# Optimization experiments

Measured on AMD Instinct MI355X. Metric: run time of the kernel, lower is better.

## Reference

```python
import jax, jax.numpy as jnp
import numpy as np

B, L, D = 8, 64, 768
F, P, A = 50, 49, 49   # frames, patches, attention dim
N, C = 20000, 36       # grid points, grid_size**2 cells
LN_EPS = 1e-12


def setup_inputs() -> dict:
    key = jax.random.key(0)
    ks = jax.random.split(key, 16)
    s = 0.02
    return {
        "lang": jax.random.normal(ks[0], (B, L, D), jnp.float32),
        "lang_cls": jax.random.normal(ks[1], (B, A), jnp.float32),
        "frames": jax.random.normal(ks[2], (B, F, P, A), jnp.float32),
        "candidates": jax.random.normal(ks[3], (B, C, 2), jnp.float32),
        "grid_fts": jax.random.normal(ks[4], (B, N, D), jnp.float32),
        "grid_index": jax.random.randint(ks[5], (B, N), 0, C, jnp.int32),
        # SoftDotAttention params (bias=False in torch)
        "W_in": jax.random.normal(ks[6], (A, A), jnp.float32) * s,
        "W_out": jax.random.normal(ks[7], (A, 2 * A), jnp.float32) * s,
        # fc2: 49 -> demb
        "W_fc2": jax.random.normal(ks[8], (D, A), jnp.float32) * s,
        "b_fc2": jnp.zeros((D,), jnp.float32),
        # text_proj / grid_proj: 768 -> 768
        "W_text": jax.random.normal(ks[9], (D, D), jnp.float32) * s,
        "b_text": jnp.zeros((D,), jnp.float32),
        "W_grid": jax.random.normal(ks[10], (D, D), jnp.float32) * s,
        "b_grid": jnp.zeros((D,), jnp.float32),
        # candidate_encoder: Linear(2, demb) + LayerNorm(demb)
        "W_cand": jax.random.normal(ks[11], (D, 2), jnp.float32) * s,
        "b_cand": jnp.zeros((D,), jnp.float32),
        "ln_g": jnp.ones((D,), jnp.float32),
        "ln_b": jnp.zeros((D,), jnp.float32),
    }


def reference(lang, lang_cls, frames, candidates, grid_fts, grid_index,
              W_in, W_out, W_fc2, b_fc2, W_text, b_text, W_grid, b_grid,
              W_cand, b_cand, ln_g, ln_b):
    # ---- SoftDotAttention over every frame (vectorized over F) ----
    target = lang_cls @ W_in.T                                  # [B,A]
    attn = jnp.einsum('bfpa,ba->bfp', frames, target)           # [B,F,P]
    attn = jax.nn.softmax(attn, axis=-1)
    wctx = jnp.einsum('bfp,bfpa->bfa', attn, frames)            # [B,F,A]
    h = jnp.broadcast_to(lang_cls[:, None, :], wctx.shape)      # [B,F,A]
    att_frame = jnp.tanh(jnp.concatenate([wctx, h], -1) @ W_out.T)  # [B,F,A]
    emb_frames = att_frame @ W_fc2.T + b_fc2                    # [B,F,D]

    # ---- grid segment softmax-reduce ----
    text = lang @ W_text.T + b_text                             # [B,L,D]
    # score of each grid point = max over language tokens
    w = jnp.einsum('bnd,bld->bnl', grid_fts, text).max(-1)      # [B,N]
    g = grid_fts @ W_grid.T + b_grid                            # [B,N,D]
    mask = grid_index[..., None] == jnp.arange(C)[None, None]   # [B,N,C]
    logits = jnp.where(mask, w[..., None], -jnp.inf)            # [B,N,C]
    m = logits.max(axis=1, keepdims=True)                       # [B,1,C]
    m = jnp.where(jnp.isfinite(m), m, 0.0)
    e = jnp.where(mask, jnp.exp(logits - m), 0.0)
    den = e.sum(axis=1, keepdims=True)                          # [B,1,C]
    p = jnp.where(den > 0, e / jnp.maximum(den, 1e-30), 0.0)    # [B,N,C]
    grid_map = jnp.einsum('bnc,bnd->bcd', p, g)                 # [B,C,D]

    # ---- candidate encoder: Linear + LayerNorm, scaled by lang[:, :1, :] ----
    c = candidates @ W_cand.T + b_cand                          # [B,C,D]
    mu = c.mean(-1, keepdims=True)
    var = ((c - mu) ** 2).mean(-1, keepdims=True)
    c = (c - mu) * jax.lax.rsqrt(var + LN_EPS) * ln_g + ln_b
    emb_cand = c * lang[:, :1, :] + grid_map                    # [B,C,D]

    return jnp.concatenate([emb_frames, emb_cand], axis=1)      # [B,F+C,D]
```

## Files before the change

### kernel.cpp

```cpp
#include <hip/hip_runtime.h>
#include <math.h>

#define Bh 8
#define Lh 64
#define Dh 768
#define Fh 50
#define Ph 49
#define Ah 49
#define Nh 20000
#define Ch 36
#define CAP 2048
#define NCH 8
#define CUTE 2e-6f

typedef __bf16 bf16x8 __attribute__((ext_vector_type(8)));
typedef float f32x4 __attribute__((ext_vector_type(4)));
union U { uint4 u; bf16x8 v; };

__device__ __forceinline__ void cvt2(float a0, float a1, unsigned& h, unsigned& l) {
    unsigned u0 = __float_as_uint(a0), u1 = __float_as_uint(a1);
    unsigned h0 = u0 & 0xFFFF0000u, h1 = u1 & 0xFFFF0000u;
    h = (h0 >> 16) | h1;
    float l0 = a0 - __uint_as_float(h0);
    float l1 = a1 - __uint_as_float(h1);
    l = (__float_as_uint(l0) >> 16) | (__float_as_uint(l1) & 0xFFFF0000u);
}

__device__ __forceinline__ void cvt8(float4 p, float4 q, bf16x8& h8, bf16x8& l8) {
    U h, l;
    cvt2(p.x, p.y, h.u.x, l.u.x);
    cvt2(p.z, p.w, h.u.y, l.u.y);
    cvt2(q.x, q.y, h.u.z, l.u.z);
    cvt2(q.z, q.w, h.u.w, l.u.w);
    h8 = h.v; l8 = l.v;
}

__device__ __forceinline__ float dec_max(unsigned u) {
    if (u == 0u) return 0.f;
    return (u & 0x80000000u) ? __uint_as_float(u ^ 0x80000000u) : __uint_as_float(~u);
}

__global__ __launch_bounds__(256) void k_prep(const float* __restrict__ Wg,
                                              const float* __restrict__ Wt,
                                              const float* __restrict__ Wf2,
                                              uint4* __restrict__ WgH, uint4* __restrict__ WgL,
                                              uint4* __restrict__ WtH, uint4* __restrict__ WtL,
                                              float* __restrict__ Wf2T,
                                              unsigned* __restrict__ m_u,
                                              float* __restrict__ den,
                                              int* __restrict__ cnt) {
    int bx = blockIdx.x, tid = threadIdx.x;
    if (bx < 576) {
        bool g = bx < 288;
        int gid = (g ? bx : bx - 288) * 256 + tid;
        const float* W = g ? Wg : Wt;
        int l = gid & 63;
        int rest = gid >> 6;
        int ct = rest % 48, ks = rest / 48;
        const float* src = W + (size_t)(ct * 16 + (l & 15)) * Dh + ks * 32 + (l >> 4) * 8;
        float4 p = *(const float4*)src;
        float4 q = *(const float4*)(src + 4);
        U h, lo;
        cvt2(p.x, p.y, h.u.x, lo.u.x);
        cvt2(p.z, p.w, h.u.y, lo.u.y);
        cvt2(q.x, q.y, h.u.z, lo.u.z);
        cvt2(q.z, q.w, h.u.w, lo.u.w);
        if (g) { WgH[gid] = h.u; WgL[gid] = lo.u; }
        else   { WtH[gid] = h.u; WtL[gid] = lo.u; }
    } else if (bx < 723) {
        int i = (bx - 576) * 256 + tid;
        int d = i / 49, j = i - d * 49;
        Wf2T[j * Dh + d] = Wf2[i];
    } else {
        for (int i = tid; i < Bh * Ch; i += 256) { m_u[i] = 0u; den[i] = 0.f; cnt[i] = 0; }
    }
}

__global__ __launch_bounds__(256) void k_tf(const float* __restrict__ lang,
                                            const uint4* __restrict__ WtH,
                                            const uint4* __restrict__ WtL,
                                            const float* __restrict__ bt,
                                            const float* __restrict__ frames,
                                            const float* __restrict__ lang_cls,
                                            const float* __restrict__ W_in,
                                            const float* __restrict__ W_out,
                                            const float* __restrict__ Wf2T,
                                            const float* __restrict__ b_fc2,
                                            float* __restrict__ text,
                                            float* __restrict__ out) {
    __shared__ float smem[8192];
    int bx = blockIdx.x;
    int tid = threadIdx.x;

    if (bx < 48) {
        float (*lds)[4096] = (float(*)[4096])smem;
        int wv = tid >> 6, l = tid & 63;
        int dt = bx % 12;
        int m0 = (bx / 12) * 128;

        const uint4* pbh = WtH + (size_t)dt * 256 + l;
        const uint4* pbl = WtL + (size_t)dt * 256 + l;

        const float* srcA[4]; int dA[4];
#pragma unroll
        for (int r = 0; r < 4; ++r) {
            int s = r * 256 + tid, row = s >> 3, pos = s & 7;
            srcA[r] = lang + (size_t)(m0 + row) * Dh + pos * 4;
            dA[r] = row * 32 + ((pos ^ (row & 7)) << 2);
        }
        int lm = l & 15, lh = l >> 4, r7 = lm & 7;
        int oA[2][2];
#pragma unroll
        for (int rt = 0; rt < 2; ++rt)
#pragma unroll
            for (int j = 0; j < 2; ++j)
                oA[rt][j] = (wv * 32 + rt * 16 + lm) * 32 + (((lh * 2 + j) ^ r7) << 2);

        {
            float4 v0 = *(const float4*)srcA[0];
            float4 v1 = *(const float4*)srcA[1];
            float4 v2 = *(const float4*)srcA[2];
            float4 v3 = *(const float4*)srcA[3];
            *(float4*)&lds[0][dA[0]] = v0;
            *(float4*)&lds[0][dA[1]] = v1;
            *(float4*)&lds[0][dA[2]] = v2;
            *(float4*)&lds[0][dA[3]] = v3;
        }
        __syncthreads();

        f32x4 acc[2][4];
#pragma unroll
        for (int i = 0; i < 2; ++i)
#pragma unroll
            for (int j = 0; j < 4; ++j) acc[i][j] = (f32x4){0.f, 0.f, 0.f, 0.f};

        for (int t = 0; t < 24; ++t) {
            int cur = t & 1;
            float4 p0, p1, p2, p3;
            bool pf = (t < 23);
            if (pf) {
                int o = (t + 1) * 32;
                p0 = *(const float4*)(srcA[0] + o);
                p1 = *(const float4*)(srcA[1] + o);
                p2 = *(const float4*)(srcA[2] + o);
                p3 = *(const float4*)(srcA[3] + o);
            }
            uint4 bh0 = pbh[t * 3072 +   0], bh1 = pbh[t * 3072 +  64];
            uint4 bh2 = pbh[t * 3072 + 128], bh3 = pbh[t * 3072 + 192];
            uint4 bl0 = pbl[t * 3072 +   0], bl1 = pbl[t * 3072 +  64];
            uint4 bl2 = pbl[t * 3072 + 128], bl3 = pbl[t * 3072 + 192];

            const float* L = lds[cur];
            float4 a00 = *(const float4*)&L[oA[0][0]];
            float4 a01 = *(const float4*)&L[oA[0][1]];
            float4 a10 = *(const float4*)&L[oA[1][0]];
            float4 a11 = *(const float4*)&L[oA[1][1]];
            bf16x8 ah0, al0, ah1, al1;
            cvt8(a00, a01, ah0, al0);
            cvt8(a10, a11, ah1, al1);

            uint4 bhu[4] = {bh0, bh1, bh2, bh3};
            uint4 blu[4] = {bl0, bl1, bl2, bl3};
#pragma unroll
            for (int ct = 0; ct < 4; ++ct) {
                U ubh, ubl; ubh.u = bhu[ct]; ubl.u = blu[ct];
                bf16x8 bh = ubh.v, bl = ubl.v;
                acc[0][ct] = __builtin_amdgcn_mfma_f32_16x16x32_bf16(ah0, bh, acc[0][ct], 0, 0, 0);
                acc[0][ct] = __builtin_amdgcn_mfma_f32_16x16x32_bf16(al0, bh, acc[0][ct], 0, 0, 0);
                acc[0][ct] = __builtin_amdgcn_mfma_f32_16x16x32_bf16(ah0, bl, acc[0][ct], 0, 0, 0);
                acc[1][ct] = __builtin_amdgcn_mfma_f32_16x16x32_bf16(ah1, bh, acc[1][ct], 0, 0, 0);
                acc[1][ct] = __builtin_amdgcn_mfma_f32_16x16x32_bf16(al1, bh, acc[1][ct], 0, 0, 0);
                acc[1][ct] = __builtin_amdgcn_mfma_f32_16x16x32_bf16(ah1, bl, acc[1][ct], 0, 0, 0);
            }
            if (pf) {
                float* D = lds[cur ^ 1];
                *(float4*)&D[dA[0]] = p0;
                *(float4*)&D[dA[1]] = p1;
                *(float4*)&D[dA[2]] = p2;
                *(float4*)&D[dA[3]] = p3;
            }
            __syncthreads();
        }

#pragma unroll
        for (int rt = 0; rt < 2; ++rt) {
#pragma unroll
            for (int r = 0; r < 4; ++r) {
                int row = m0 + wv * 32 + rt * 16 + lh * 4 + r;
#pragma unroll
                for (int ct = 0; ct < 4; ++ct) {
                    int d = dt * 64 + ct * 16 + lm;
                    text[(size_t)row * Dh + d] = acc[rt][ct][r] + bt[d];
                }
            }
        }
    } else {
        int fid = bx - 48;
        int b = fid / Fh, f = fid % Fh;
        float* fr = smem;
        float* tg = smem + 2401;
        float* cl = smem + 2450;
        float* at = smem + 2499;
        float* wc = smem + 2548;
        float* af = smem + 2597;
        const float* fp = frames + ((size_t)(b * Fh + f)) * (Ph * Ah);
        for (int i = tid; i < Ph * Ah; i += 256) fr[i] = fp[i];
        if (tid < Ah) {
            cl[tid] = lang_cls[b * Ah + tid];
            float s = 0.f;
            for (int k = 0; k < Ah; ++k) s += lang_cls[b * Ah + k] * W_in[tid * Ah + k];
            tg[tid] = s;
        }
        __syncthreads();
        if (tid < Ph) {
            float s = 0.f;
            for (int a = 0; a < Ah; ++a) s += fr[tid * Ah + a] * tg[a];
            at[tid] = s;
        }
        __syncthreads();
        if (tid < 64) {
            float raw = (tid < Ph) ? at[tid] : -3.4e38f;
            float v = raw;
            for (int m = 32; m; m >>= 1) v = fmaxf(v, __shfl_xor(v, m));
            float e = (tid < Ph) ? expf(raw - v) : 0.f;
            float s = e;
            for (int m = 32; m; m >>= 1) s += __shfl_xor(s, m);
            if (tid < Ph) at[tid] = e / s;
        }
        __syncthreads();
        if (tid < Ah) {
            float s = 0.f;
            for (int p = 0; p < Ph; ++p) s += at[p] * fr[p * Ah + tid];
            wc[tid] = s;
        }
        __syncthreads();
        if (tid < Ah) {
            float s = 0.f;
            for (int a = 0; a < Ah; ++a)
                s += wc[a] * W_out[tid * (2 * Ah) + a] + cl[a] * W_out[tid * (2 * Ah) + Ah + a];
            af[tid] = tanhf(s);
        }
        __syncthreads();
        for (int d = tid; d < Dh; d += 256) {
            float s = b_fc2[d];
            for (int j = 0; j < Ah; ++j) s += af[j] * Wf2T[j * Dh + d];
            out[((size_t)(b * (Fh + Ch) + f)) * Dh + d] = s;
        }
    }
}

__global__ __launch_bounds__(256) void k_tfrag(const float* __restrict__ text,
                                               uint4* __restrict__ textH,
                                               uint4* __restrict__ textL) {
    int gid = blockIdx.x * 256 + threadIdx.x;
    int l  = gid & 63;
    int ct = (gid >> 6) & 3;
    int bk = gid >> 8;
    int b  = bk / 24, ks = bk % 24;
    const float* src = text + ((size_t)(b * Lh + ct * 16 + (l & 15))) * Dh
                     + ks * 32 + (l >> 4) * 8;
    float4 p = *(const float4*)src;
    float4 q = *(const float4*)(src + 4);
    U h, lo;
    cvt2(p.x, p.y, h.u.x, lo.u.x);
    cvt2(p.z, p.w, h.u.y, lo.u.y);
    cvt2(q.x, q.y, h.u.z, lo.u.z);
    cvt2(q.z, q.w, h.u.w, lo.u.w);
    textH[gid] = h.u;
    textL[gid] = lo.u;
}

__global__ __launch_bounds__(256) void k_w(const float* __restrict__ grid,
                                           const uint4* __restrict__ textH,
                                           const uint4* __restrict__ textL,
                                           const int* __restrict__ gi,
                                           float* __restrict__ w,
                                           unsigned* __restrict__ m_u) {
    __shared__ float lds[2][4096];
    __shared__ unsigned mu[Ch];
    int b = blockIdx.y;
    int tid = threadIdx.x;
    int wv = tid >> 6, l = tid & 63;
    int n0 = blockIdx.x * 128;
    if (tid < Ch) mu[tid] = 0u;

    const float* gb = grid + (size_t)b * Nh * Dh;
    const uint4* pbh = textH + (size_t)b * 6144 + l;
    const uint4* pbl = textL + (size_t)b * 6144 + l;

    const float* srcA[4]; int dA[4];
#pragma unroll
    for (int r = 0; r < 4; ++r) {
        int s = r * 256 + tid, row = s >> 3, pos = s & 7;
        int rowg = n0 + row; if (rowg >= Nh) rowg = Nh - 1;
        srcA[r] = gb + (size_t)rowg * Dh + pos * 4;
        dA[r] = row * 32 + ((pos ^ (row & 7)) << 2);
    }
    int lm = l & 15, lh = l >> 4, r7 = lm & 7;
    int oA[2][2];
#pragma unroll
    for (int rt = 0; rt < 2; ++rt)
#pragma unroll
        for (int j = 0; j < 2; ++j)
            oA[rt][j] = (wv * 32 + rt * 16 + lm) * 32 + (((lh * 2 + j) ^ r7) << 2);

    {
        float4 v0 = *(const float4*)srcA[0];
        float4 v1 = *(const float4*)srcA[1];
        float4 v2 = *(const float4*)srcA[2];
        float4 v3 = *(const float4*)srcA[3];
        *(float4*)&lds[0][dA[0]] = v0;
        *(float4*)&lds[0][dA[1]] = v1;
        *(float4*)&lds[0][dA[2]] = v2;
        *(float4*)&lds[0][dA[3]] = v3;
    }
    __syncthreads();

    f32x4 acc[2][4];
#pragma unroll
    for (int i = 0; i < 2; ++i)
#pragma unroll
        for (int j = 0; j < 4; ++j) acc[i][j] = (f32x4){0.f, 0.f, 0.f, 0.f};

    for (int t = 0; t < 24; ++t) {
        int cur = t & 1;
        float4 p0, p1, p2, p3;
        bool pf = (t < 23);
        if (pf) {
            int o = (t + 1) * 32;
            p0 = *(const float4*)(srcA[0] + o);
            p1 = *(const float4*)(srcA[1] + o);
            p2 = *(const float4*)(srcA[2] + o);
            p3 = *(const float4*)(srcA[3] + o);
        }
        uint4 bh0 = pbh[t * 256 +   0], bh1 = pbh[t * 256 +  64];
        uint4 bh2 = pbh[t * 256 + 128], bh3 = pbh[t * 256 + 192];
        uint4 bl0 = pbl[t * 256 +   0], bl1 = pbl[t * 256 +  64];
        uint4 bl2 = pbl[t * 256 + 128], bl3 = pbl[t * 256 + 192];

        const float* L = lds[cur];
        float4 a00 = *(const float4*)&L[oA[0][0]];
        float4 a01 = *(const float4*)&L[oA[0][1]];
        float4 a10 = *(const float4*)&L[oA[1][0]];
        float4 a11 = *(const float4*)&L[oA[1][1]];
        bf16x8 ah0, al0, ah1, al1;
        cvt8(a00, a01, ah0, al0);
        cvt8(a10, a11, ah1, al1);

        uint4 bhu[4] = {bh0, bh1, bh2, bh3};
        uint4 blu[4] = {bl0, bl1, bl2, bl3};
#pragma unroll
        for (int ct = 0; ct < 4; ++ct) {
            U ubh, ubl; ubh.u = bhu[ct]; ubl.u = blu[ct];
            bf16x8 bh = ubh.v, bl = ubl.v;
            acc[0][ct] = __builtin_amdgcn_mfma_f32_16x16x32_bf16(ah0, bh, acc[0][ct], 0, 0, 0);
            acc[0][ct] = __builtin_amdgcn_mfma_f32_16x16x32_bf16(al0, bh, acc[0][ct], 0, 0, 0);
            acc[0][ct] = __builtin_amdgcn_mfma_f32_16x16x32_bf16(ah0, bl, acc[0][ct], 0, 0, 0);
            acc[1][ct] = __builtin_amdgcn_mfma_f32_16x16x32_bf16(ah1, bh, acc[1][ct], 0, 0, 0);
            acc[1][ct] = __builtin_amdgcn_mfma_f32_16x16x32_bf16(al1, bh, acc[1][ct], 0, 0, 0);
            acc[1][ct] = __builtin_amdgcn_mfma_f32_16x16x32_bf16(ah1, bl, acc[1][ct], 0, 0, 0);
        }
        if (pf) {
            float* D = lds[cur ^ 1];
            *(float4*)&D[dA[0]] = p0;
            *(float4*)&D[dA[1]] = p1;
            *(float4*)&D[dA[2]] = p2;
            *(float4*)&D[dA[3]] = p3;
        }
        __syncthreads();
    }

#pragma unroll
    for (int rt = 0; rt < 2; ++rt) {
        float m[4];
#pragma unroll
        for (int r = 0; r < 4; ++r) {
            m[r] = fmaxf(fmaxf(acc[rt][0][r], acc[rt][1][r]),
                         fmaxf(acc[rt][2][r], acc[rt][3][r]));
            m[r] = fmaxf(m[r], __shfl_xor(m[r], 1));
            m[r] = fmaxf(m[r], __shfl_xor(m[r], 2));
            m[r] = fmaxf(m[r], __shfl_xor(m[r], 4));
            m[r] = fmaxf(m[r], __shfl_xor(m[r], 8));
        }
        if (lm == 0) {
#pragma unroll
            for (int r = 0; r < 4; ++r) {
                int row = n0 + wv * 32 + rt * 16 + lh * 4 + r;
                if (row < Nh) {
                    w[b * Nh + row] = m[r];
                    unsigned u = __float_as_uint(m[r]);
                    u = (u & 0x80000000u) ? ~u : (u | 0x80000000u);
                    atomicMax(&mu[gi[b * Nh + row]], u);
                }
            }
        }
    }
    __syncthreads();
    if (tid < Ch && mu[tid]) atomicMax(&m_u[b * Ch + tid], mu[tid]);
}

__global__ __launch_bounds__(256) void k_epc(const float* __restrict__ w,
                                             const int* __restrict__ gi,
                                             const unsigned* __restrict__ m_u,
                                             float* __restrict__ den,
                                             int* __restrict__ cnt,
                                             int* __restrict__ bn,
                                             float* __restrict__ bp) {
    int b = blockIdx.y;
    int n = blockIdx.x * 256 + threadIdx.x;
    __shared__ float dn[Ch];
    if (threadIdx.x < Ch) dn[threadIdx.x] = 0.f;
    __syncthreads();
    if (n < Nh) {
        int c = gi[b * Nh + n];
        float e = expf(w[b * Nh + n] - dec_max(m_u[b * Ch + c]));
        atomicAdd(&dn[c], e);
        if (e > CUTE) {
            int pos = atomicAdd(&cnt[b * Ch + c], 1);
            if (pos < CAP) {
                bn[(b * Ch + c) * CAP + pos] = n;
                bp[(b * Ch + c) * CAP + pos] = e;
            }
        }
    }
    __syncthreads();
    if (threadIdx.x < Ch && dn[threadIdx.x] != 0.f)
        atomicAdd(&den[b * Ch + threadIdx.x], dn[threadIdx.x]);
}

__global__ __launch_bounds__(256) void k_S3(const float* __restrict__ grid,
                                            const int* __restrict__ cnt,
                                            const int* __restrict__ bn,
                                            const float* __restrict__ bp,
                                            float* __restrict__ Spart) {
    int c = blockIdx.x, dq = blockIdx.y;
    int b = blockIdx.z >> 3, ch = blockIdx.z & 7;
    int d = dq * 256 + threadIdx.x;
    int len = cnt[b * Ch + c]; if (len > CAP) len = CAP;
    int i0 = ch * (CAP / NCH);
    int i1 = i0 + (CAP / NCH); if (i1 > len) i1 = len;
    size_t base = (size_t)(b * Ch + c) * CAP;
    size_t po = ((size_t)(b * Ch + c) * NCH + ch) * Dh + d;
    const float* gb = grid + (size_t)b * Nh * Dh + d;
    float a[8] = {0.f, 0.f, 0.f, 0.f, 0.f, 0.f, 0.f, 0.f};
    int i = i0;
    for (; i + 8 <= i1; i += 8) {
        int nn[8]; float pp[8];
#pragma unroll
        for (int j = 0; j < 8; ++j) { nn[j] = bn[base + i + j]; pp[j] = bp[base + i + j]; }
#pragma unroll
        for (int j = 0; j < 8; ++j) a[j] += pp[j] * gb[(size_t)nn[j] * Dh];
    }
    for (; i < i1; ++i) a[0] += bp[base + i] * gb[(size_t)bn[base + i] * Dh];
    Spart[po] = ((a[0] + a[1]) + (a[2] + a[3])) + ((a[4] + a[5]) + (a[6] + a[7]));
}

__global__ __launch_bounds__(256) void k_red(const float* __restrict__ Spart,
                                             float* __restrict__ S) {
    int bc = blockIdx.x, dq = blockIdx.y;
    int d = dq * 256 + threadIdx.x;
    float s = 0.f;
#pragma unroll
    for (int ch = 0; ch < NCH; ++ch)
        s += Spart[((size_t)bc * NCH + ch) * Dh + d];
    S[(size_t)bc * Dh + d] = s;
}

__global__ __launch_bounds__(256) void k_gg2(const float* __restrict__ S,
                                             const float* __restrict__ den,
                                             const uint4* __restrict__ WgH,
                                             const uint4* __restrict__ WgL,
                                             const float* __restrict__ bg,
                                             float* __restrict__ G) {
    __shared__ float lds[2][4096];
    int tid = threadIdx.x;
    int wv = tid >> 6, l = tid & 63;
    int m0 = blockIdx.y * 128;
    int dt = blockIdx.x;

    const uint4* pbh = WgH + (size_t)dt * 256 + l;
    const uint4* pbl = WgL + (size_t)dt * 256 + l;

    const float* srcA[4]; int dA[4];
#pragma unroll
    for (int r = 0; r < 4; ++r) {
        int s = r * 256 + tid, row = s >> 3, pos = s & 7;
        int rowg = m0 + row; if (rowg >= Bh * Ch) rowg = Bh * Ch - 1;
        srcA[r] = S + (size_t)rowg * Dh + pos * 4;
        dA[r] = row * 32 + ((pos ^ (row & 7)) << 2);
    }
    int lm = l & 15, lh = l >> 4, r7 = lm & 7;
    int oA[2][2];
#pragma unroll
    for (int rt = 0; rt < 2; ++rt)
#pragma unroll
        for (int j = 0; j < 2; ++j)
            oA[rt][j] = (wv * 32 + rt * 16 + lm) * 32 + (((lh * 2 + j) ^ r7) << 2);

    {
        float4 v0 = *(const float4*)srcA[0];
        float4 v1 = *(const float4*)srcA[1];
        float4 v2 = *(const float4*)srcA[2];
        float4 v3 = *(const float4*)srcA[3];
        *(float4*)&lds[0][dA[0]] = v0;
        *(float4*)&lds[0][dA[1]] = v1;
        *(float4*)&lds[0][dA[2]] = v2;
        *(float4*)&lds[0][dA[3]] = v3;
    }
    __syncthreads();

    f32x4 acc[2][4];
#pragma unroll
    for (int i = 0; i < 2; ++i)
#pragma unroll
        for (int j = 0; j < 4; ++j) acc[i][j] = (f32x4){0.f, 0.f, 0.f, 0.f};

    for (int t = 0; t < 24; ++t) {
        int cur = t & 1;
        float4 p0, p1, p2, p3;
        bool pf = (t < 23);
        if (pf) {
            int o = (t + 1) * 32;
            p0 = *(const float4*)(srcA[0] + o);
            p1 = *(const float4*)(srcA[1] + o);
            p2 = *(const float4*)(srcA[2] + o);
            p3 = *(const float4*)(srcA[3] + o);
        }
        uint4 bh0 = pbh[t * 3072 +   0], bh1 = pbh[t * 3072 +  64];
        uint4 bh2 = pbh[t * 3072 + 128], bh3 = pbh[t * 3072 + 192];
        uint4 bl0 = pbl[t * 3072 +   0], bl1 = pbl[t * 3072 +  64];
        uint4 bl2 = pbl[t * 3072 + 128], bl3 = pbl[t * 3072 + 192];

        const float* L = lds[cur];
        float4 a00 = *(const float4*)&L[oA[0][0]];
        float4 a01 = *(const float4*)&L[oA[0][1]];
        float4 a10 = *(const float4*)&L[oA[1][0]];
        float4 a11 = *(const float4*)&L[oA[1][1]];
        bf16x8 ah0, al0, ah1, al1;
        cvt8(a00, a01, ah0, al0);
        cvt8(a10, a11, ah1, al1);

        uint4 bhu[4] = {bh0, bh1, bh2, bh3};
        uint4 blu[4] = {bl0, bl1, bl2, bl3};
#pragma unroll
        for (int ct = 0; ct < 4; ++ct) {
            U ubh, ubl; ubh.u = bhu[ct]; ubl.u = blu[ct];
            bf16x8 bh = ubh.v, bl = ubl.v;
            acc[0][ct] = __builtin_amdgcn_mfma_f32_16x16x32_bf16(ah0, bh, acc[0][ct], 0, 0, 0);
            acc[0][ct] = __builtin_amdgcn_mfma_f32_16x16x32_bf16(al0, bh, acc[0][ct], 0, 0, 0);
            acc[0][ct] = __builtin_amdgcn_mfma_f32_16x16x32_bf16(ah0, bl, acc[0][ct], 0, 0, 0);
            acc[1][ct] = __builtin_amdgcn_mfma_f32_16x16x32_bf16(ah1, bh, acc[1][ct], 0, 0, 0);
            acc[1][ct] = __builtin_amdgcn_mfma_f32_16x16x32_bf16(al1, bh, acc[1][ct], 0, 0, 0);
            acc[1][ct] = __builtin_amdgcn_mfma_f32_16x16x32_bf16(ah1, bl, acc[1][ct], 0, 0, 0);
        }
        if (pf) {
            float* D = lds[cur ^ 1];
            *(float4*)&D[dA[0]] = p0;
            *(float4*)&D[dA[1]] = p1;
            *(float4*)&D[dA[2]] = p2;
            *(float4*)&D[dA[3]] = p3;
        }
        __syncthreads();
    }

#pragma unroll
    for (int rt = 0; rt < 2; ++rt) {
#pragma unroll
        for (int r = 0; r < 4; ++r) {
            int row = m0 + wv * 32 + rt * 16 + lh * 4 + r;
            if (row < Bh * Ch) {
                float dv = den[row];
                float inv = (dv > 0.f) ? 1.f / dv : 0.f;
#pragma unroll
                for (int ct = 0; ct < 4; ++ct) {
                    int d = dt * 64 + ct * 16 + lm;
                    G[(size_t)row * Dh + d] = acc[rt][ct][r] * inv + bg[d];
                }
            }
        }
    }
}

__global__ __launch_bounds__(256) void k_final(const float* __restrict__ G,
                                               const float* __restrict__ den,
                                               const float* __restrict__ cands,
                                               const float* __restrict__ W_cand,
                                               const float* __restrict__ b_cand,
                                               const float* __restrict__ ln_g,
                                               const float* __restrict__ ln_b,
                                               const float* __restrict__ lang,
                                               float* __restrict__ out) {
    int b = blockIdx.x / Ch, c = blockIdx.x % Ch;
    int tid = threadIdx.x;
    __shared__ float cv[Dh];
    __shared__ float red[8];
    __shared__ float mu_s, rs_s;
    float cx = cands[(b * Ch + c) * 2 + 0], cy = cands[(b * Ch + c) * 2 + 1];
    for (int d = tid; d < Dh; d += 256)
        cv[d] = W_cand[d * 2] * cx + W_cand[d * 2 + 1] * cy + b_cand[d];
    __syncthreads();
    float ls = 0.f;
    for (int d = tid; d < Dh; d += 256) ls += cv[d];
    for (int m = 32; m; m >>= 1) ls += __shfl_xor(ls, m);
    if ((tid & 63) == 0) red[tid >> 6] = ls;
    __syncthreads();
    if (tid == 0) mu_s = (red[0] + red[1] + red[2] + red[3]) * (1.f / Dh);
    __syncthreads();
    float mu = mu_s;
    float lv = 0.f;
    for (int d = tid; d < Dh; d += 256) { float t = cv[d] - mu; lv += t * t; }
    for (int m = 32; m; m >>= 1) lv += __shfl_xor(lv, m);
    if ((tid & 63) == 0) red[4 + (tid >> 6)] = lv;
    __syncthreads();
    if (tid == 0) rs_s = rsqrtf((red[4] + red[5] + red[6] + red[7]) * (1.f / Dh) + 1e-12f);
    __syncthreads();
    float rs = rs_s;
    float dv = den[b * Ch + c];
#pragma unroll
    for (int j = 0; j < 3; ++j) {
        int d = tid + j * 256;
        float gm = (dv > 0.f) ? G[(size_t)(b * Ch + c) * Dh + d] : 0.f;
        float cn = (cv[d] - mu) * rs * ln_g[d] + ln_b[d];
        out[((size_t)(b * (Fh + Ch) + Fh + c)) * Dh + d] =
            cn * lang[((size_t)b * Lh) * Dh + d] + gm;
    }
}

extern "C" void kernel_launch(void* const* d_in, const int* in_sizes, int n_in,
                              void* d_out, int out_size, void* d_ws, size_t ws_size,
                              hipStream_t stream) {
    (void)in_sizes; (void)n_in; (void)out_size; (void)ws_size;
    const float* lang      = (const float*)d_in[0];
    const float* lang_cls  = (const float*)d_in[1];
    const float* frames    = (const float*)d_in[2];
    const float* cands     = (const float*)d_in[3];
    const float* grid_fts  = (const float*)d_in[4];
    const int*   grid_idx  = (const int*)d_in[5];
    const float* W_in      = (const float*)d_in[6];
    const float* W_out     = (const float*)d_in[7];
    const float* W_fc2     = (const float*)d_in[8];
    const float* b_fc2     = (const float*)d_in[9];
    const float* W_text    = (const float*)d_in[10];
    const float* b_text    = (const float*)d_in[11];
    const float* W_grid    = (const float*)d_in[12];
    const float* b_grid    = (const float*)d_in[13];
    const float* W_cand    = (const float*)d_in[14];
    const float* b_cand    = (const float*)d_in[15];
    const float* ln_g      = (const float*)d_in[16];
    const float* ln_b      = (const float*)d_in[17];
    float* out = (float*)d_out;
    float* ws  = (float*)d_ws;

    float*    wbuf  = ws;
    unsigned* m_u   = (unsigned*)(ws + 160000);
    float*    den   = ws + 160288;
    int*      cnt   = (int*)(ws + 160576);
    int*      bn    = (int*)(ws + 160864);
    float*    bp    = ws + 750688;
    float*    Spart = ws + 1340512;
    float*    G     = ws + 3109984;
    uint4*    textH = (uint4*)(ws + 3331168);
    uint4*    textL = (uint4*)(ws + 3527776);
    float*    S     = ws + 3724384;
    uint4*    WgH   = (uint4*)(ws + 3945568);
    uint4*    WgL   = (uint4*)(ws + 4240480);
    uint4*    WtH   = (uint4*)(ws + 4535392);
    uint4*    WtL   = (uint4*)(ws + 4830304);
    float*    Wf2T  = ws + 5125216;
    float*    text  = ws + 5162848;

    hipLaunchKernelGGL(k_prep,   dim3(724), dim3(256), 0, stream,
                       W_grid, W_text, W_fc2, WgH, WgL, WtH, WtL, Wf2T, m_u, den, cnt);
    hipLaunchKernelGGL(k_tf,     dim3(448), dim3(256), 0, stream,
                       lang, WtH, WtL, b_text, frames, lang_cls, W_in, W_out, Wf2T, b_fc2,
                       text, out);
    hipLaunchKernelGGL(k_tfrag,  dim3(192), dim3(256), 0, stream, text, textH, textL);
    hipLaunchKernelGGL(k_w,      dim3((Nh + 127) / 128, Bh), dim3(256), 0, stream,
                       grid_fts, textH, textL, grid_idx, wbuf, m_u);
    hipLaunchKernelGGL(k_epc,    dim3(79, Bh), dim3(256), 0, stream,
                       wbuf, grid_idx, m_u, den, cnt, bn, bp);
    hipLaunchKernelGGL(k_S3,     dim3(Ch, 3, Bh * NCH), dim3(256), 0, stream,
                       grid_fts, cnt, bn, bp, Spart);
    hipLaunchKernelGGL(k_red,    dim3(Bh * Ch, 3), dim3(256), 0, stream, Spart, S);
    hipLaunchKernelGGL(k_gg2,    dim3(12, 3), dim3(256), 0, stream,
                       S, den, WgH, WgL, b_grid, G);
    hipLaunchKernelGGL(k_final,  dim3(Bh * Ch), dim3(256), 0, stream,
                       G, den, cands, W_cand, b_cand, ln_g, ln_b, lang, out);
}
```

Measured before the change: 226.3 us.

## Fuse partial-sum reduction and final epilogue into grid GEMM, move LayerNorm to prep

Removes the k_red and k_final launches. The grid-projection GEMM now sums the NCH partial slices directly while loading its A tiles, and writes the final candidate output itself using a precomputed LayerNorm result. The candidate Linear+LayerNorm moves into extra blocks of the prep kernel, whose output is stored in the buffer G used to occupy. This cuts two launches and the S/G round trips, but each GEMM A-tile load now reads 8 partial slices. That extra load work lands in a kernel with only 36 blocks.

```diff
diff --git a/kernel.cpp b/kernel.cpp
--- a/kernel.cpp
+++ b/kernel.cpp
@@ -40,15 +40,34 @@
     return (u & 0x80000000u) ? __uint_as_float(u ^ 0x80000000u) : __uint_as_float(~u);
 }
 
+__device__ __forceinline__ float4 sumS(const float* __restrict__ Spart, int rowg, int d) {
+    float4 s = {0.f, 0.f, 0.f, 0.f};
+#pragma unroll
+    for (int ch = 0; ch < NCH; ++ch) {
+        float4 v = *(const float4*)&Spart[((size_t)rowg * NCH + ch) * Dh + d];
+        s.x += v.x; s.y += v.y; s.z += v.z; s.w += v.w;
+    }
+    return s;
+}
+
 __global__ __launch_bounds__(256) void k_prep(const float* __restrict__ Wg,
                                               const float* __restrict__ Wt,
                                               const float* __restrict__ Wf2,
+                                              const float* __restrict__ cands,
+                                              const float* __restrict__ W_cand,
+                                              const float* __restrict__ b_cand,
+                                              const float* __restrict__ ln_g,
+                                              const float* __restrict__ ln_b,
                                               uint4* __restrict__ WgH, uint4* __restrict__ WgL,
                                               uint4* __restrict__ WtH, uint4* __restrict__ WtL,
                                               float* __restrict__ Wf2T,
+                                              float* __restrict__ cn,
                                               unsigned* __restrict__ m_u,
                                               float* __restrict__ den,
                                               int* __restrict__ cnt) {
+    __shared__ float cv[Dh];
+    __shared__ float red[8];
+    __shared__ float mu_s, rs_s;
     int bx = blockIdx.x, tid = threadIdx.x;
     if (bx < 576) {
         bool g = bx < 288;
@@ -71,8 +90,36 @@
         int i = (bx - 576) * 256 + tid;
         int d = i / 49, j = i - d * 49;
         Wf2T[j * Dh + d] = Wf2[i];
+    } else if (bx == 723) {
+        for (int i = tid; i < Bh * Ch; i += 256) { m_u[i] = 0u; den[i] = 0.f; cnt[i] = 0; }
     } else {
-        for (int i = tid; i < Bh * Ch; i += 256) { m_u[i] = 0u; den[i] = 0.f; cnt[i] = 0; }
+        int idx = bx - 724;
+        int b = idx / Ch, c = idx % Ch;
+        float cx = cands[(b * Ch + c) * 2 + 0], cy = cands[(b * Ch + c) * 2 + 1];
+        for (int d = tid; d < Dh; d += 256)
+            cv[d] = W_cand[d * 2] * cx + W_cand[d * 2 + 1] * cy + b_cand[d];
+        __syncthreads();
+        float ls = 0.f;
+        for (int d = tid; d < Dh; d += 256) ls += cv[d];
+        for (int m = 32; m; m >>= 1) ls += __shfl_xor(ls, m);
+        if ((tid & 63) == 0) red[tid >> 6] = ls;
+        __syncthreads();
+        if (tid == 0) mu_s = (red[0] + red[1] + red[2] + red[3]) * (1.f / Dh);
+        __syncthreads();
+        float mu = mu_s;
+        float lv = 0.f;
+        for (int d = tid; d < Dh; d += 256) { float t = cv[d] - mu; lv += t * t; }
+        for (int m = 32; m; m >>= 1) lv += __shfl_xor(lv, m);
+        if ((tid & 63) == 0) red[4 + (tid >> 6)] = lv;
+        __syncthreads();
+        if (tid == 0) rs_s = rsqrtf((red[4] + red[5] + red[6] + red[7]) * (1.f / Dh) + 1e-12f);
+        __syncthreads();
+        float rs = rs_s;
+#pragma unroll
+        for (int j = 0; j < 3; ++j) {
+            int d = tid + j * 256;
+            cn[(size_t)(b * Ch + c) * Dh + d] = (cv[d] - mu) * rs * ln_g[d] + ln_b[d];
+        }
     }
 }
 
@@ -455,23 +502,14 @@
     Spart[po] = ((a[0] + a[1]) + (a[2] + a[3])) + ((a[4] + a[5]) + (a[6] + a[7]));
 }
 
-__global__ __launch_bounds__(256) void k_red(const float* __restrict__ Spart,
-                                             float* __restrict__ S) {
-    int bc = blockIdx.x, dq = blockIdx.y;
-    int d = dq * 256 + threadIdx.x;
-    float s = 0.f;
-#pragma unroll
-    for (int ch = 0; ch < NCH; ++ch)
-        s += Spart[((size_t)bc * NCH + ch) * Dh + d];
-    S[(size_t)bc * Dh + d] = s;
-}
-
-__global__ __launch_bounds__(256) void k_gg2(const float* __restrict__ S,
+__global__ __launch_bounds__(256) void k_gg2(const float* __restrict__ Spart,
                                              const float* __restrict__ den,
                                              const uint4* __restrict__ WgH,
                                              const uint4* __restrict__ WgL,
                                              const float* __restrict__ bg,
-                                             float* __restrict__ G) {
+                                             const float* __restrict__ cn,
+                                             const float* __restrict__ lang,
+                                             float* __restrict__ out) {
     __shared__ float lds[2][4096];
     int tid = threadIdx.x;
     int wv = tid >> 6, l = tid & 63;
@@ -481,12 +519,12 @@
     const uint4* pbh = WgH + (size_t)dt * 256 + l;
     const uint4* pbl = WgL + (size_t)dt * 256 + l;
 
-    const float* srcA[4]; int dA[4];
+    int rowgA[4], posA[4], dA[4];
 #pragma unroll
     for (int r = 0; r < 4; ++r) {
         int s = r * 256 + tid, row = s >> 3, pos = s & 7;
         int rowg = m0 + row; if (rowg >= Bh * Ch) rowg = Bh * Ch - 1;
-        srcA[r] = S + (size_t)rowg * Dh + pos * 4;
+        rowgA[r] = rowg; posA[r] = pos * 4;
         dA[r] = row * 32 + ((pos ^ (row & 7)) << 2);
     }
     int lm = l & 15, lh = l >> 4, r7 = lm & 7;
@@ -498,10 +536,10 @@
             oA[rt][j] = (wv * 32 + rt * 16 + lm) * 32 + (((lh * 2 + j) ^ r7) << 2);
 
     {
-        float4 v0 = *(const float4*)srcA[0];
-        float4 v1 = *(const float4*)srcA[1];
-        float4 v2 = *(const float4*)srcA[2];
-        float4 v3 = *(const float4*)srcA[3];
+        float4 v0 = sumS(Spart, rowgA[0], posA[0]);
+        float4 v1 = sumS(Spart, rowgA[1], posA[1]);
+        float4 v2 = sumS(Spart, rowgA[2], posA[2]);
+        float4 v3 = sumS(Spart, rowgA[3], posA[3]);
         *(float4*)&lds[0][dA[0]] = v0;
         *(float4*)&lds[0][dA[1]] = v1;
         *(float4*)&lds[0][dA[2]] = v2;
@@ -521,10 +559,10 @@
         bool pf = (t < 23);
         if (pf) {
             int o = (t + 1) * 32;
-            p0 = *(const float4*)(srcA[0] + o);
-            p1 = *(const float4*)(srcA[1] + o);
-            p2 = *(const float4*)(srcA[2] + o);
-            p3 = *(const float4*)(srcA[3] + o);
+            p0 = sumS(Spart, rowgA[0], posA[0] + o);
+            p1 = sumS(Spart, rowgA[1], posA[1] + o);
+            p2 = sumS(Spart, rowgA[2], posA[2] + o);
+            p3 = sumS(Spart, rowgA[3], posA[3] + o);
         }
         uint4 bh0 = pbh[t * 3072 +   0], bh1 = pbh[t * 3072 +  64];
         uint4 bh2 = pbh[t * 3072 + 128], bh3 = pbh[t * 3072 + 192];
@@ -571,58 +609,17 @@
             if (row < Bh * Ch) {
                 float dv = den[row];
                 float inv = (dv > 0.f) ? 1.f / dv : 0.f;
+                int bb = row / Ch, cc = row - bb * Ch;
+                const float* lrow = lang + (size_t)bb * Lh * Dh;
 #pragma unroll
                 for (int ct = 0; ct < 4; ++ct) {
                     int d = dt * 64 + ct * 16 + lm;
-                    G[(size_t)row * Dh + d] = acc[rt][ct][r] * inv + bg[d];
+                    float gm = (dv > 0.f) ? acc[rt][ct][r] * inv + bg[d] : 0.f;
+                    out[((size_t)(bb * (Fh + Ch) + Fh + cc)) * Dh + d] =
+                        cn[(size_t)row * Dh + d] * lrow[d] + gm;
                 }
             }
         }
-    }
-}
-
-__global__ __launch_bounds__(256) void k_final(const float* __restrict__ G,
-                                               const float* __restrict__ den,
-                                               const float* __restrict__ cands,
-                                               const float* __restrict__ W_cand,
-                                               const float* __restrict__ b_cand,
-                                               const float* __restrict__ ln_g,
-                                               const float* __restrict__ ln_b,
-                                               const float* __restrict__ lang,
-                                               float* __restrict__ out) {
-    int b = blockIdx.x / Ch, c = blockIdx.x % Ch;
-    int tid = threadIdx.x;
-    __shared__ float cv[Dh];
-    __shared__ float red[8];
-    __shared__ float mu_s, rs_s;
-    float cx = cands[(b * Ch + c) * 2 + 0], cy = cands[(b * Ch + c) * 2 + 1];
-    for (int d = tid; d < Dh; d += 256)
-        cv[d] = W_cand[d * 2] * cx + W_cand[d * 2 + 1] * cy + b_cand[d];
-    __syncthreads();
-    float ls = 0.f;
-    for (int d = tid; d < Dh; d += 256) ls += cv[d];
-    for (int m = 32; m; m >>= 1) ls += __shfl_xor(ls, m);
-    if ((tid & 63) == 0) red[tid >> 6] = ls;
-    __syncthreads();
-    if (tid == 0) mu_s = (red[0] + red[1] + red[2] + red[3]) * (1.f / Dh);
-    __syncthreads();
-    float mu = mu_s;
-    float lv = 0.f;
-    for (int d = tid; d < Dh; d += 256) { float t = cv[d] - mu; lv += t * t; }
-    for (int m = 32; m; m >>= 1) lv += __shfl_xor(lv, m);
-    if ((tid & 63) == 0) red[4 + (tid >> 6)] = lv;
-    __syncthreads();
-    if (tid == 0) rs_s = rsqrtf((red[4] + red[5] + red[6] + red[7]) * (1.f / Dh) + 1e-12f);
-    __syncthreads();
-    float rs = rs_s;
-    float dv = den[b * Ch + c];
-#pragma unroll
-    for (int j = 0; j < 3; ++j) {
-        int d = tid + j * 256;
-        float gm = (dv > 0.f) ? G[(size_t)(b * Ch + c) * Dh + d] : 0.f;
-        float cn = (cv[d] - mu) * rs * ln_g[d] + ln_b[d];
-        out[((size_t)(b * (Fh + Ch) + Fh + c)) * Dh + d] =
-            cn * lang[((size_t)b * Lh) * Dh + d] + gm;
     }
 }
 
@@ -658,10 +655,9 @@
     int*      bn    = (int*)(ws + 160864);
     float*    bp    = ws + 750688;
     float*    Spart = ws + 1340512;
-    float*    G     = ws + 3109984;
+    float*    cn    = ws + 3109984;
     uint4*    textH = (uint4*)(ws + 3331168);
     uint4*    textL = (uint4*)(ws + 3527776);
-    float*    S     = ws + 3724384;
     uint4*    WgH   = (uint4*)(ws + 3945568);
     uint4*    WgL   = (uint4*)(ws + 4240480);
     uint4*    WtH   = (uint4*)(ws + 4535392);
@@ -669,8 +665,9 @@
     float*    Wf2T  = ws + 5125216;
     float*    text  = ws + 5162848;
 
-    hipLaunchKernelGGL(k_prep,   dim3(724), dim3(256), 0, stream,
-                       W_grid, W_text, W_fc2, WgH, WgL, WtH, WtL, Wf2T, m_u, den, cnt);
+    hipLaunchKernelGGL(k_prep,   dim3(1012), dim3(256), 0, stream,
+                       W_grid, W_text, W_fc2, cands, W_cand, b_cand, ln_g, ln_b,
+                       WgH, WgL, WtH, WtL, Wf2T, cn, m_u, den, cnt);
     hipLaunchKernelGGL(k_tf,     dim3(448), dim3(256), 0, stream,
                        lang, WtH, WtL, b_text, frames, lang_cls, W_in, W_out, Wf2T, b_fc2,
                        text, out);
@@ -681,9 +678,6 @@
                        wbuf, grid_idx, m_u, den, cnt, bn, bp);
     hipLaunchKernelGGL(k_S3,     dim3(Ch, 3, Bh * NCH), dim3(256), 0, stream,
                        grid_fts, cnt, bn, bp, Spart);
-    hipLaunchKernelGGL(k_red,    dim3(Bh * Ch, 3), dim3(256), 0, stream, Spart, S);
     hipLaunchKernelGGL(k_gg2,    dim3(12, 3), dim3(256), 0, stream,
-                       S, den, WgH, WgL, b_grid, G);
-    hipLaunchKernelGGL(k_final,  dim3(Bh * Ch), dim3(256), 0, stream,
-                       G, den, cands, W_cand, b_cand, ln_g, ln_b, lang, out);
-}
+                       Spart, den, WgH, WgL, b_grid, cn, lang, out);
+}
```

Result: slower. 329.2 us (+45.4%).
